# Performance work log

Hardware: AMD Instinct MI355X
Metric: run time of the kernel (lower is better)

Reference implementation:

```python
import jax, jax.numpy as jnp
import numpy as np

# dims (match init_kwargs)
T, B, N, D_OB = 256, 32, 64, 4
D_MODEL = N * D_OB            # 256
D_PE = 16
D_T = D_MODEL + D_PE          # 272 transformer width
H = 8
DH = D_T // H                 # 34
L = 2
DFF = 1024
C = 2
MAX_LEN = T
F_IN = T * D_OB               # 1024, ObservationPropagation channels


def setup_inputs() -> dict:
    key = jax.random.key(0)
    ks = jax.random.split(key, 24)
    g = lambda k, shp: 0.02 * jax.random.normal(k, shp, dtype=jnp.float32)
    return {
        "x": jax.random.normal(ks[0], (T, B, N), dtype=jnp.float32),
        "times": jnp.sort(jax.random.uniform(ks[1], (T, B), dtype=jnp.float32) * MAX_LEN, axis=0),
        "lengths": jax.random.randint(ks[2], (B,), MAX_LEN // 2, MAX_LEN + 1),
        "R_u": g(ks[3], (1, N * D_OB)),
        "Wv1": g(ks[4], (F_IN, F_IN)), "bv1": g(ks[5], (F_IN,)),
        "Wv2": g(ks[6], (F_IN, F_IN)), "bv2": g(ks[7], (F_IN,)),
        "qkv_w": g(ks[8], (L, D_T, 3 * D_T)), "qkv_b": g(ks[9], (L, 3 * D_T)),
        "out_w": g(ks[10], (L, D_T, D_T)), "out_b": g(ks[11], (L, D_T)),
        "ln1_w": jnp.ones((L, D_T), jnp.float32), "ln1_b": jnp.zeros((L, D_T), jnp.float32),
        "ln2_w": jnp.ones((L, D_T), jnp.float32), "ln2_b": jnp.zeros((L, D_T), jnp.float32),
        "ffn_w1": g(ks[12], (L, D_T, DFF)), "ffn_b1": g(ks[13], (L, DFF)),
        "ffn_w2": g(ks[14], (L, DFF, D_T)), "ffn_b2": g(ks[15], (L, D_T)),
        "mlp_w1": g(ks[16], (D_T, D_T)), "mlp_b1": g(ks[17], (D_T,)),
        "mlp_w2": g(ks[18], (D_T, C)), "mlp_b2": g(ks[19], (C,)),
    }


def _pos_encode(times):
    # PositionalEncodingTF: timescales = max_len ** linspace(0,1,d_pe//2)
    scales = MAX_LEN ** np.linspace(0.0, 1.0, D_PE // 2)
    st = times[..., None] / jnp.asarray(scales, times.dtype)  # [T,B,8]
    return jnp.concatenate([jnp.sin(st), jnp.cos(st)], axis=-1)  # [T,B,16]


def _segment_softmax(w, seg, num_segments):
    m = jax.ops.segment_max(w, seg, num_segments=num_segments)
    e = jnp.exp(w - m[seg])
    s = jax.ops.segment_sum(e, seg, num_segments=num_segments)
    return e / s[seg]


def _ob_propagate(xn, src, tgt, edge_w, Wv, bv):
    """Batched ObservationPropagation (use_beta=False, decompose=False).
    xn: [B,N,F]; messages = relu(lin_value(x_src)) * softmax(edge_w per target);
    scatter-add at targets. Returns (out, pre-softmax alpha == edge_w)."""
    gamma = _segment_softmax(edge_w, tgt, N)              # [E]
    value = jax.nn.relu(xn @ Wv + bv)                     # [B,N,F] (linear commutes with gather)
    msg = value[:, src, :] * gamma[None, :, None]         # [B,E,F] -- dominant memory traffic
    out = jnp.zeros_like(xn).at[:, tgt, :].add(msg)       # segment-sum at target nodes
    return out, edge_w


def _ln(x, w, b):
    mu = jnp.mean(x, axis=-1, keepdims=True)
    var = jnp.mean((x - mu) ** 2, axis=-1, keepdims=True)
    return (x - mu) / jnp.sqrt(var + 1e-5) * w + b


def _encoder_layer(xt, key_pad, qkv_w, qkv_b, out_w, out_b, ln1_w, ln1_b, ln2_w, ln2_b, w1, b1, w2, b2):
    # xt: [T,B,D_T]; key_pad: [B,T] True = padded. Post-norm torch TransformerEncoderLayer, relu, no dropout.
    Tt, Bb, _ = xt.shape
    q, k, v = jnp.split(xt @ qkv_w + qkv_b, 3, axis=-1)
    to_h = lambda t: t.reshape(Tt, Bb, H, DH).transpose(1, 2, 0, 3)  # [B,H,T,dh]
    scores = jnp.einsum("bhqd,bhkd->bhqk", to_h(q), to_h(k)) / jnp.sqrt(jnp.asarray(DH, xt.dtype))
    scores = jnp.where(key_pad[:, None, None, :], -jnp.inf, scores)
    attn = jax.nn.softmax(scores, axis=-1)
    o = jnp.einsum("bhqk,bhkd->bhqd", attn, to_h(v)).transpose(2, 0, 1, 3).reshape(Tt, Bb, D_T)
    xt = _ln(xt + o @ out_w + out_b, ln1_w, ln1_b)
    ff = jax.nn.relu(xt @ w1 + b1) @ w2 + b2
    return _ln(xt + ff, ln2_w, ln2_b)


def _forward(x, times, lengths, R_u, Wv1, bv1, Wv2, bv2, qkv_w, qkv_b, out_w, out_b,
             ln1_w, ln1_b, ln2_w, ln2_b, ffn_w1, ffn_b1, ffn_w2, ffn_b2,
             mlp_w1, mlp_b1, mlp_w2, mlp_b2):
    Bb = x.shape[1]
    # observation embedding: repeat each sensor d_ob times, scale by R_u, relu
    h = jax.nn.relu(jnp.repeat(x, D_OB, axis=-1) * R_u)          # [T,B,N*d_ob]
    pe = _pos_encode(times)                                      # [T,B,16]
    key_pad = jnp.arange(T)[None, :] >= lengths[:, None]         # [B,T]
    # reshape to per-sensor node features: [B, N, T*d_ob]
    xn = h.reshape(T, Bb, N, D_OB).transpose(1, 2, 0, 3).reshape(Bb, N, F_IN)
    # dense all-pairs graph (global_structure = ones); torch.nonzero order is row-major
    src = jnp.repeat(jnp.arange(N), N)   # edge_index[0]
    tgt = jnp.tile(jnp.arange(N), N)     # edge_index[1] (aggregation index)
    ew = jnp.ones((N * N,), x.dtype)
    xn, ew2 = _ob_propagate(xn, src, tgt, ew, Wv1, bv1)
    xn, _ = _ob_propagate(xn, src, tgt, ew2, Wv2, bv2)
    out = xn.reshape(Bb, N, T, D_OB).transpose(2, 0, 1, 3).reshape(T, Bb, N * D_OB)
    out = jnp.concatenate([out, pe], axis=2)                     # [T,B,272]
    for l in range(L):
        out = _encoder_layer(out, key_pad, qkv_w[l], qkv_b[l], out_w[l], out_b[l],
                             ln1_w[l], ln1_b[l], ln2_w[l], ln2_b[l],
                             ffn_w1[l], ffn_b1[l], ffn_w2[l], ffn_b2[l])
    keep = (~key_pad).T[:, :, None].astype(out.dtype)            # [T,B,1]
    agg = jnp.sum(out * keep, axis=0) / (lengths[:, None].astype(out.dtype) + 1.0)
    hid = jax.nn.relu(agg @ mlp_w1 + mlp_b1)
    logits = hid @ mlp_w2 + mlp_b2
    return jax.nn.softmax(logits, axis=1)                        # [B,C]


def reference(x, times, lengths, R_u, Wv1, bv1, Wv2, bv2, qkv_w, qkv_b, out_w, out_b,
              ln1_w, ln1_b, ln2_w, ln2_b, ffn_w1, ffn_b1, ffn_w2, ffn_b2,
              mlp_w1, mlp_b1, mlp_w2, mlp_b2):
    return _forward(x, times, lengths, R_u, Wv1, bv1, Wv2, bv2, qkv_w, qkv_b, out_w, out_b,
                    ln1_w, ln1_b, ln2_w, ln2_b, ffn_w1, ffn_b1, ffn_w2, ffn_b2,
                    mlp_w1, mlp_b1, mlp_w2, mlp_b2)
```

## Files before the change

kernel.cpp:

```cpp
#include <hip/hip_runtime.h>
#include <math.h>

#define T_DIM 256
#define B_DIM 32
#define N_DIM 64
#define F_INF 1024
#define D_T 272
#define D_TP 288
#define H_DIM 8
#define DH_DIM 34
#define DFF_DIM 1024

typedef unsigned int uint;
typedef short bf16x8 __attribute__((ext_vector_type(8)));
typedef float f32x4 __attribute__((ext_vector_type(4)));

__device__ __forceinline__ ushort f2bf(float f) {
    uint u = __float_as_uint(f);
    uint r = (u + 0x7fffu + ((u >> 16) & 1u)) >> 16;
    return (ushort)r;
}
__device__ __forceinline__ float bf2f(ushort u) {
    return __uint_as_float(((uint)u) << 16);
}

__global__ void xn_kernel(const float* __restrict__ x, const float* __restrict__ Ru,
                          ushort* __restrict__ xn) {
    int idx = blockIdx.x * blockDim.x + threadIdx.x;
    if (idx >= B_DIM * N_DIM * F_INF) return;
    int f = idx & 1023;
    int bn = idx >> 10;
    int n = bn & 63;
    int b = bn >> 6;
    int t = f >> 2;
    int d = f & 3;
    float v = x[(t * B_DIM + b) * N_DIM + n] * Ru[(n << 2) + d];
    xn[idx] = f2bf(fmaxf(v, 0.0f));
}

struct WT {
    int tstart[11];
    const float* src[10];
    ushort* dst[10];
    int K[10];
    int N[10];
    int Kp[10];
    int ntn[10];
};
__global__ __launch_bounds__(256) void wconv_tiled(WT s) {
    int tile = blockIdx.x;
    int seg = 0;
    while (seg < 9 && tile >= s.tstart[seg + 1]) ++seg;
    int ti = tile - s.tstart[seg];
    int ntn = s.ntn[seg];
    int tk = ti / ntn, tn = ti - tk * ntn;
    int N = s.N[seg], Kp = s.Kp[seg];
    __shared__ float t[16][17];
    int ty = threadIdx.x >> 4, tx = threadIdx.x & 15;
    t[ty][tx] = s.src[seg][(size_t)(tk * 16 + ty) * N + tn * 16 + tx];
    __syncthreads();
    s.dst[seg][(size_t)(tn * 16 + ty) * Kp + tk * 16 + tx] = f2bf(t[tx][ty]);
}

template <int ACT, int OUT_MODE>
__global__ __launch_bounds__(256) void gemm_mfma(const ushort* __restrict__ A,
                                                 const ushort* __restrict__ Bt,
                                                 const float* __restrict__ bias,
                                                 void* __restrict__ Cout,
                                                 int M, int N, int K, int Kstride) {
    __shared__ ushort As[4][64 * 32];
    __shared__ ushort Bs[4][128 * 32];
    const int tid = threadIdx.x;
    const int m0 = (OUT_MODE == 3) ? 0 : blockIdx.y * 64;
    const int n0 = blockIdx.x * 128;
    if (OUT_MODE == 3) {
        A += (size_t)blockIdx.y * K;
        Bt += (size_t)blockIdx.y * K;
    }
    const int w = tid >> 6, lane = tid & 63;
    const int wr = w >> 1, wc = w & 1;
    const int lr = lane & 15, lk = lane >> 4;

    const int ns = K >> 5;

    const int ra = w * 16 + (lane >> 2);
    const int ca = (((lane & 3) ^ ((ra >> 1) & 3)) << 3);
    int gma = m0 + ra; if (gma > M - 1) gma = M - 1;
    const ushort* gA = &A[(size_t)gma * Kstride + ca];
    const int rb0 = w * 32 + (lane >> 2);
    const int cb0 = (((lane & 3) ^ ((rb0 >> 1) & 3)) << 3);
    const int rb1 = rb0 + 16;
    const int cb1 = (((lane & 3) ^ ((rb1 >> 1) & 3)) << 3);
    int gnb0 = n0 + rb0; if (gnb0 > N - 1) gnb0 = N - 1;
    int gnb1 = n0 + rb1; if (gnb1 > N - 1) gnb1 = N - 1;
    const ushort* gB0 = &Bt[(size_t)gnb0 * Kstride + cb0];
    const ushort* gB1 = &Bt[(size_t)gnb1 * Kstride + cb1];

    f32x4 acc[2][4];
#pragma unroll
    for (int i = 0; i < 2; ++i)
#pragma unroll
        for (int j = 0; j < 4; ++j) acc[i][j] = (f32x4){0.f, 0.f, 0.f, 0.f};

    auto stage = [&](int buf, int s) {
        const int k0 = s << 5;
        __builtin_amdgcn_global_load_lds(
            (const __attribute__((address_space(1))) void*)(gA + k0),
            (__attribute__((address_space(3))) void*)(&As[buf][w * 512]), 16, 0, 0);
        __builtin_amdgcn_global_load_lds(
            (const __attribute__((address_space(1))) void*)(gB0 + k0),
            (__attribute__((address_space(3))) void*)(&Bs[buf][w * 1024]), 16, 0, 0);
        __builtin_amdgcn_global_load_lds(
            (const __attribute__((address_space(1))) void*)(gB1 + k0),
            (__attribute__((address_space(3))) void*)(&Bs[buf][w * 1024 + 512]), 16, 0, 0);
    };

    stage(0, 0);
    stage(1, 1);
    stage(2, 2);
    asm volatile("s_waitcnt vmcnt(6)" ::: "memory");
    __builtin_amdgcn_sched_barrier(0);
    __builtin_amdgcn_s_barrier();
    __builtin_amdgcn_sched_barrier(0);

    int cur = 0;
    for (int s = 0; s < ns; ++s) {
        int stg = (cur + 3) & 3;
        if (s + 3 < ns) stage(stg, s + 3);

        bf16x8 af[2], bf[4];
#pragma unroll
        for (int mt = 0; mt < 2; ++mt) {
            int row = wr * 32 + mt * 16 + lr;
            int ch = lk ^ ((row >> 1) & 3);
            af[mt] = *reinterpret_cast<const bf16x8*>(&As[cur][row * 32 + ch * 8]);
        }
#pragma unroll
        for (int nt = 0; nt < 4; ++nt) {
            int row = wc * 64 + nt * 16 + lr;
            int ch = lk ^ ((row >> 1) & 3);
            bf[nt] = *reinterpret_cast<const bf16x8*>(&Bs[cur][row * 32 + ch * 8]);
        }
        __builtin_amdgcn_s_setprio(1);
#pragma unroll
        for (int mt = 0; mt < 2; ++mt)
#pragma unroll
            for (int nt = 0; nt < 4; ++nt)
                acc[mt][nt] = __builtin_amdgcn_mfma_f32_16x16x32_bf16(
                    af[mt], bf[nt], acc[mt][nt], 0, 0, 0);
        __builtin_amdgcn_s_setprio(0);

        if (s + 1 < ns) {
            if (s + 3 < ns)
                asm volatile("s_waitcnt vmcnt(6)" ::: "memory");
            else if (s + 2 < ns)
                asm volatile("s_waitcnt vmcnt(3)" ::: "memory");
            else
                asm volatile("s_waitcnt vmcnt(0)" ::: "memory");
            __builtin_amdgcn_sched_barrier(0);
            __builtin_amdgcn_s_barrier();
            __builtin_amdgcn_sched_barrier(0);
        }
        cur = (cur + 1) & 3;
    }

#pragma unroll
    for (int nt = 0; nt < 4; ++nt) {
        int col = n0 + wc * 64 + nt * 16 + lr;
        if (col >= N) continue;
        float bv = (OUT_MODE == 3) ? 0.f : bias[col];
        int g = 0, dcol = 0;
        if (OUT_MODE == 2) { g = col / 34; dcol = col - g * 34; }
#pragma unroll
        for (int mt = 0; mt < 2; ++mt) {
#pragma unroll
            for (int r = 0; r < 4; ++r) {
                int row = m0 + wr * 32 + mt * 16 + lk * 4 + r;
                if (row >= M) continue;
                float v = acc[mt][nt][r] + bv;
                if (ACT == 1) v = fmaxf(v, 0.0f);
                if (OUT_MODE == 0)
                    ((float*)Cout)[(size_t)row * N + col] = v;
                else if (OUT_MODE == 1)
                    ((ushort*)Cout)[(size_t)row * N + col] = f2bf(v);
                else if (OUT_MODE == 2)
                    ((ushort*)Cout)[(size_t)row * 960 + g * 40 + dcol] = f2bf(v);
                else
                    ((float*)Cout)[(size_t)(blockIdx.y * M + row) * N + col] = v;
            }
        }
    }
}

__global__ __launch_bounds__(256) void reduce_s1_kernel(const ushort* __restrict__ val1,
                                                        ushort* __restrict__ s1) {
    int idx = blockIdx.x * 256 + threadIdx.x;
    if (idx >= B_DIM * 128) return;
    int b = idx >> 7;
    int g0 = (idx & 127) << 3;
    const ushort* base = val1 + (size_t)(b << 6) * F_INF + g0;
    float s[8] = {0.f, 0.f, 0.f, 0.f, 0.f, 0.f, 0.f, 0.f};
    for (int n = 0; n < 64; ++n) {
        bf16x8 v = *reinterpret_cast<const bf16x8*>(base + (size_t)n * F_INF);
#pragma unroll
        for (int e = 0; e < 8; ++e) s[e] += bf2f((ushort)v[e]);
    }
    ushort o[8];
#pragma unroll
    for (int e = 0; e < 8; ++e) o[e] = f2bf(s[e] * (1.0f / 64.0f));
    *reinterpret_cast<uint4*>(&s1[(size_t)idx * 8]) = *reinterpret_cast<uint4*>(o);
}

__global__ __launch_bounds__(256) void reduce_p2_kernel(const float* __restrict__ part,
                                                        const float* __restrict__ bv2,
                                                        float* __restrict__ out2) {
    int idx = blockIdx.x * 256 + threadIdx.x;
    if (idx >= B_DIM * F_INF) return;
    int g = idx & 1023;
    float s = bv2[g];
#pragma unroll
    for (int ks = 0; ks < 4; ++ks) s += part[(size_t)ks * B_DIM * F_INF + idx];
    out2[idx] = fmaxf(s, 0.f);
}

__global__ void seq_kernel(const float* __restrict__ out2, const float* __restrict__ times,
                           ushort* __restrict__ seq) {
    int idx = blockIdx.x * blockDim.x + threadIdx.x;
    if (idx >= T_DIM * B_DIM * D_TP) return;
    int c = idx % D_TP;
    int tb = idx / D_TP;
    float v;
    if (c < 256) {
        v = out2[(tb % B_DIM) * 1024 + ((tb / B_DIM) << 2) + (c & 3)];
    } else if (c < 272) {
        int s = c - 256;
        int sc = (s < 8) ? s : s - 8;
        float arg = times[tb] * exp2f(-8.0f * (float)sc * (1.0f / 7.0f));
        v = (s < 8) ? sinf(arg) : cosf(arg);
    } else {
        v = 0.f;
    }
    seq[idx] = f2bf(v);
}

struct PadPtrs {
    uint* wt[6];
    int nrows[6];
};
__global__ void init_pads_kernel(uint* __restrict__ qkvb, uint* __restrict__ x1,
                                 uint* __restrict__ attno, PadPtrs p) {
    const int TB = T_DIM * B_DIM;
    int idx = blockIdx.x * blockDim.x + threadIdx.x;
    if (idx < TB * 8) {
        int row = idx >> 3, q = idx & 7;
        x1[(size_t)row * 144 + 136 + q] = 0;
        attno[(size_t)row * 144 + 136 + q] = 0;
        return;
    }
    idx -= TB * 8;
    if (idx < TB * 72) {
        int row = idx / 72;
        int r = idx - row * 72;
        int g = r / 3, q = r - g * 3;
        qkvb[(size_t)row * 480 + g * 20 + 17 + q] = 0;
        return;
    }
    idx -= TB * 72;
#pragma unroll
    for (int sgi = 0; sgi < 6; ++sgi) {
        int cnt = p.nrows[sgi] * 8;
        if (idx < cnt) {
            int row = idx >> 3, q = idx & 7;
            p.wt[sgi][(size_t)row * 144 + 136 + q] = 0;
            return;
        }
        idx -= cnt;
    }
}

__global__ __launch_bounds__(256) void attn_mfma(const ushort* __restrict__ qkv,
                                                 const int* __restrict__ lengths,
                                                 ushort* __restrict__ attno) {
    const int b = blockIdx.x >> 3;
    const int h = blockIdx.x & 7;
    const int tid = threadIdx.x;
    const int w = tid >> 6, lane = tid & 63;
    const int lr = lane & 15, lk = lane >> 4;
    __shared__ ushort Ks[2][64 * 40];
    __shared__ ushort Vt[2][48 * 72];
    __shared__ ushort Ps[4][64 * 72];
    const int len = lengths[b];
    const float scale = 0.1714985851f;
    const bf16x8 zv = {0, 0, 0, 0, 0, 0, 0, 0};

    for (int i = tid; i < 2 * 8 * 72; i += 256) {
        int bb = i / 576;
        Vt[bb][40 * 72 + (i - bb * 576)] = 0;
    }

    const int srow0 = tid / 5, sch0 = tid - srow0 * 5;
    const int srow1 = (tid + 256) / 5, sch1 = (tid + 256) - srow1 * 5;
    const int sjp0 = (srow0 & 15) * 4 + (srow0 >> 4);
    const int sjp1 = (srow1 & 15) * 4 + (srow1 >> 4);
    const bool has1 = (tid < 64);
    bf16x8 kreg0, kreg1, vreg0, vreg1;

    auto LOADS = [&](int c) {
        const ushort* b0 = &qkv[(size_t)((c * 64 + srow0) * 32 + b) * 960 + h * 40];
        kreg0 = *reinterpret_cast<const bf16x8*>(b0 + 320 + sch0 * 8);
        vreg0 = *reinterpret_cast<const bf16x8*>(b0 + 640 + sch0 * 8);
        if (has1) {
            const ushort* b1 = &qkv[(size_t)((c * 64 + srow1) * 32 + b) * 960 + h * 40];
            kreg1 = *reinterpret_cast<const bf16x8*>(b1 + 320 + sch1 * 8);
            vreg1 = *reinterpret_cast<const bf16x8*>(b1 + 640 + sch1 * 8);
        }
    };
    auto WRITES = [&](int buf) {
        *reinterpret_cast<bf16x8*>(&Ks[buf][srow0 * 40 + sch0 * 8]) = kreg0;
#pragma unroll
        for (int e = 0; e < 8; ++e) Vt[buf][(sch0 * 8 + e) * 72 + sjp0] = (ushort)vreg0[e];
        if (has1) {
            *reinterpret_cast<bf16x8*>(&Ks[buf][srow1 * 40 + sch1 * 8]) = kreg1;
#pragma unroll
            for (int e = 0; e < 8; ++e) Vt[buf][(sch1 * 8 + e) * 72 + sjp1] = (ushort)vreg1[e];
        }
    };

    bf16x8 qf0[4], qf1[4];
#pragma unroll
    for (int it = 0; it < 4; ++it) {
        int t = w * 64 + it * 16 + lr;
        const ushort* qrow = &qkv[(size_t)(t * 32 + b) * 960 + h * 40];
        qf0[it] = *reinterpret_cast<const bf16x8*>(qrow + lk * 8);
        qf1[it] = (lk == 0) ? *reinterpret_cast<const bf16x8*>(qrow + 32) : zv;
    }

    f32x4 oacc[4][3];
#pragma unroll
    for (int it = 0; it < 4; ++it)
#pragma unroll
        for (int dt = 0; dt < 3; ++dt) oacc[it][dt] = (f32x4){0.f, 0.f, 0.f, 0.f};
    float m[4][4], l[4][4];
#pragma unroll
    for (int it = 0; it < 4; ++it)
#pragma unroll
        for (int r = 0; r < 4; ++r) { m[it][r] = -1e30f; l[it][r] = 0.f; }

    const int nchunks = (len + 63) >> 6;
    LOADS(0);
    WRITES(0);
    __syncthreads();

    int cur = 0;
    for (int c = 0; c < nchunks; ++c) {
        const bool pre = (c + 1 < nchunks);
        if (pre) LOADS(c + 1);

        bf16x8 kf0[4], kf1[4];
#pragma unroll
        for (int jt = 0; jt < 4; ++jt) {
            int j = jt * 16 + lr;
            kf0[jt] = *reinterpret_cast<const bf16x8*>(&Ks[cur][j * 40 + lk * 8]);
            kf1[jt] = (lk == 0) ? *reinterpret_cast<const bf16x8*>(&Ks[cur][j * 40 + 32]) : zv;
        }

        const bool tail = (c * 64 + 64 > len);
#pragma unroll
        for (int it = 0; it < 4; ++it) {
            f32x4 sacc[4];
#pragma unroll
            for (int jt = 0; jt < 4; ++jt) sacc[jt] = (f32x4){0.f, 0.f, 0.f, 0.f};
            __builtin_amdgcn_s_setprio(1);
#pragma unroll
            for (int jt = 0; jt < 4; ++jt) {
                sacc[jt] = __builtin_amdgcn_mfma_f32_16x16x32_bf16(qf0[it], kf0[jt],
                                                                   sacc[jt], 0, 0, 0);
                sacc[jt] = __builtin_amdgcn_mfma_f32_16x16x32_bf16(qf1[it], kf1[jt],
                                                                   sacc[jt], 0, 0, 0);
            }
            __builtin_amdgcn_s_setprio(0);
            float cm[4] = {-1e30f, -1e30f, -1e30f, -1e30f};
#pragma unroll
            for (int jt = 0; jt < 4; ++jt) {
                bool dead = tail && (c * 64 + jt * 16 + lr >= len);
#pragma unroll
                for (int r = 0; r < 4; ++r) {
                    float sv = dead ? -1e30f : sacc[jt][r];
                    sacc[jt][r] = sv;
                    cm[r] = fmaxf(cm[r], sv);
                }
            }
#pragma unroll
            for (int mask = 1; mask <= 8; mask <<= 1)
#pragma unroll
                for (int r = 0; r < 4; ++r) cm[r] = fmaxf(cm[r], __shfl_xor(cm[r], mask));
#pragma unroll
            for (int r = 0; r < 4; ++r) {
                float mn = fmaxf(m[it][r], cm[r]);
                float corr = __expf((m[it][r] - mn) * scale);
                m[it][r] = mn;
                l[it][r] *= corr;
#pragma unroll
                for (int dt = 0; dt < 3; ++dt) oacc[it][dt][r] *= corr;
            }
            float ls[4] = {0.f, 0.f, 0.f, 0.f};
#pragma unroll
            for (int jt = 0; jt < 4; ++jt)
#pragma unroll
                for (int r = 0; r < 4; ++r) {
                    float e = __expf((sacc[jt][r] - m[it][r]) * scale);
                    sacc[jt][r] = e;
                    ls[r] += e;
                }
#pragma unroll
            for (int mask = 1; mask <= 8; mask <<= 1)
#pragma unroll
                for (int r = 0; r < 4; ++r) ls[r] += __shfl_xor(ls[r], mask);
#pragma unroll
            for (int r = 0; r < 4; ++r) l[it][r] += ls[r];
#pragma unroll
            for (int r = 0; r < 4; ++r) {
                int i = it * 16 + lk * 4 + r;
                uint u0 = (uint)f2bf(sacc[0][r]) | ((uint)f2bf(sacc[1][r]) << 16);
                uint u1 = (uint)f2bf(sacc[2][r]) | ((uint)f2bf(sacc[3][r]) << 16);
                uint2 pk = make_uint2(u0, u1);
                *reinterpret_cast<uint2*>(&Ps[w][i * 72 + lr * 4]) = pk;
            }
        }

        bf16x8 vf[3][2], pf[4][2];
#pragma unroll
        for (int dt = 0; dt < 3; ++dt)
#pragma unroll
            for (int ks = 0; ks < 2; ++ks)
                vf[dt][ks] = *reinterpret_cast<const bf16x8*>(
                    &Vt[cur][(dt * 16 + lr) * 72 + ks * 32 + lk * 8]);
#pragma unroll
        for (int it = 0; it < 4; ++it)
#pragma unroll
            for (int ks = 0; ks < 2; ++ks)
                pf[it][ks] = *reinterpret_cast<const bf16x8*>(
                    &Ps[w][(it * 16 + lr) * 72 + ks * 32 + lk * 8]);
        __builtin_amdgcn_s_setprio(1);
#pragma unroll
        for (int it = 0; it < 4; ++it)
#pragma unroll
            for (int dt = 0; dt < 3; ++dt)
#pragma unroll
                for (int ks = 0; ks < 2; ++ks)
                    oacc[it][dt] = __builtin_amdgcn_mfma_f32_16x16x32_bf16(
                        pf[it][ks], vf[dt][ks], oacc[it][dt], 0, 0, 0);
        __builtin_amdgcn_s_setprio(0);

        if (pre) WRITES(cur ^ 1);
        __syncthreads();
        cur ^= 1;
    }

#pragma unroll
    for (int it = 0; it < 4; ++it)
#pragma unroll
        for (int r = 0; r < 4; ++r) {
            float inv = 1.0f / l[it][r];
            int t = w * 64 + it * 16 + lk * 4 + r;
            ushort* orow = &attno[(size_t)(t * 32 + b) * D_TP + h * 34];
#pragma unroll
            for (int dt = 0; dt < 3; ++dt) {
                int d = dt * 16 + lr;
                if (d < 34) orow[d] = f2bf(oacc[it][dt][r] * inv);
            }
        }
}

__global__ __launch_bounds__(256) void ln_kernel(const ushort* __restrict__ X,
                                                 const float* __restrict__ Y,
                                                 const float* __restrict__ w,
                                                 const float* __restrict__ bsh,
                                                 ushort* __restrict__ out) {
    int row = blockIdx.x * 4 + (threadIdx.x >> 6);
    int lane = threadIdx.x & 63;
    const ushort* xr = X + (size_t)row * D_TP;
    const float* yr = Y + (size_t)row * D_T;
    float v[5];
    float sum = 0.f, sumsq = 0.f;
#pragma unroll
    for (int k = 0; k < 5; ++k) {
        int c = lane + k * 64;
        float t = 0.f;
        if (c < D_T) t = bf2f(xr[c]) + yr[c];
        v[k] = t;
        sum += t;
        sumsq += t * t;
    }
#pragma unroll
    for (int off = 32; off; off >>= 1) {
        sum += __shfl_down(sum, off);
        sumsq += __shfl_down(sumsq, off);
    }
    sum = __shfl(sum, 0);
    sumsq = __shfl(sumsq, 0);
    float mu = sum * (1.0f / D_T);
    float var = sumsq * (1.0f / D_T) - mu * mu;
    float inv = 1.0f / sqrtf(var + 1e-5f);
    ushort* orow = out + (size_t)row * D_TP;
#pragma unroll
    for (int k = 0; k < 5; ++k) {
        int c = lane + k * 64;
        if (c < D_T) orow[c] = f2bf((v[k] - mu) * inv * w[c] + bsh[c]);
    }
}

__global__ __launch_bounds__(256) void pool_partial(const ushort* __restrict__ seq,
                                                    const int* __restrict__ lengths,
                                                    float* __restrict__ partial) {
    const int chunk = blockIdx.x;
    const int b = blockIdx.y;
    const int tid = threadIdx.x;
    if (tid >= 136) return;
    const int len = lengths[b];
    float s0 = 0.f, s1 = 0.f;
    int t0 = chunk * 32;
    int tmax = len - t0;
    if (tmax > 32) tmax = 32;
#pragma unroll 4
    for (int r = 0; r < tmax; ++r) {
        uint u = *reinterpret_cast<const uint*>(
            &seq[(size_t)((t0 + r) * B_DIM + b) * D_TP + tid * 2]);
        s0 += __uint_as_float(u << 16);
        s1 += __uint_as_float(u & 0xffff0000u);
    }
    float* p = &partial[(size_t)(chunk * B_DIM + b) * D_T + tid * 2];
    p[0] = s0;
    p[1] = s1;
}

__global__ __launch_bounds__(256) void head_kernel(const float* __restrict__ partial,
                                                   const int* __restrict__ lengths,
                                                   const float* __restrict__ w1,
                                                   const float* __restrict__ b1,
                                                   const float* __restrict__ w2,
                                                   const float* __restrict__ b2,
                                                   float* __restrict__ out) {
    const int b = blockIdx.x;
    const int tid = threadIdx.x;
    const int len = lengths[b];
    __shared__ float agg_s[D_T];
    __shared__ float hid[D_T];
    float inv = 1.0f / (float)(len + 1);
    for (int c = tid; c < D_T; c += 256) {
        float s = 0.f;
#pragma unroll
        for (int ch = 0; ch < 8; ++ch)
            s += partial[(size_t)(ch * B_DIM + b) * D_T + c];
        agg_s[c] = s * inv;
    }
    __syncthreads();
    for (int j = tid; j < D_T; j += 256) {
        float acc = b1[j];
        for (int k = 0; k < D_T; ++k) acc += agg_s[k] * w1[k * D_T + j];
        hid[j] = fmaxf(acc, 0.f);
    }
    __syncthreads();
    if (tid < 64) {
        float l0 = 0.f, l1 = 0.f;
        for (int k = tid; k < D_T; k += 64) {
            float hv = hid[k];
            l0 += hv * w2[k * 2 + 0];
            l1 += hv * w2[k * 2 + 1];
        }
#pragma unroll
        for (int off = 32; off; off >>= 1) {
            l0 += __shfl_down(l0, off);
            l1 += __shfl_down(l1, off);
        }
        if (tid == 0) {
            l0 += b2[0];
            l1 += b2[1];
            float mx = fmaxf(l0, l1);
            float e0 = expf(l0 - mx), e1 = expf(l1 - mx);
            float nrm = 1.0f / (e0 + e1);
            out[b * 2 + 0] = e0 * nrm;
            out[b * 2 + 1] = e1 * nrm;
        }
    }
}

extern "C" void kernel_launch(void* const* d_in, const int* in_sizes, int n_in,
                              void* d_out, int out_size, void* d_ws, size_t ws_size,
                              hipStream_t stream) {
    const float* x      = (const float*)d_in[0];
    const float* times  = (const float*)d_in[1];
    const int*   lens   = (const int*)d_in[2];
    const float* R_u    = (const float*)d_in[3];
    const float* Wv1    = (const float*)d_in[4];
    const float* bv1    = (const float*)d_in[5];
    const float* Wv2    = (const float*)d_in[6];
    const float* bv2    = (const float*)d_in[7];
    const float* qkv_w  = (const float*)d_in[8];
    const float* qkv_b  = (const float*)d_in[9];
    const float* out_w  = (const float*)d_in[10];
    const float* out_b  = (const float*)d_in[11];
    const float* ln1_w  = (const float*)d_in[12];
    const float* ln1_b  = (const float*)d_in[13];
    const float* ln2_w  = (const float*)d_in[14];
    const float* ln2_b  = (const float*)d_in[15];
    const float* ffn_w1 = (const float*)d_in[16];
    const float* ffn_b1 = (const float*)d_in[17];
    const float* ffn_w2 = (const float*)d_in[18];
    const float* ffn_b2 = (const float*)d_in[19];
    const float* mlp_w1 = (const float*)d_in[20];
    const float* mlp_b1 = (const float*)d_in[21];
    const float* mlp_w2 = (const float*)d_in[22];
    const float* mlp_b2 = (const float*)d_in[23];
    float* outp = (float*)d_out;

    char* base = (char*)d_ws;
    size_t used = 0;
    auto alloc = [&](size_t bytes) -> char* {
        char* p = base + used;
        used += (bytes + 255) & ~(size_t)255;
        return p;
    };
    const int TB = T_DIM * B_DIM;

    ushort* xn    = (ushort*)alloc((size_t)2048 * 1024 * 2);
    ushort* val1  = (ushort*)alloc((size_t)2048 * 1024 * 2);
    ushort* s1    = (ushort*)alloc((size_t)32 * 1024 * 2);
    float*  p2p   = (float*) alloc((size_t)4 * 32 * 1024 * 4);
    float*  out2  = (float*) alloc((size_t)32 * 1024 * 4);
    ushort* seq   = (ushort*)alloc((size_t)TB * D_TP * 2);
    ushort* qkvb  = (ushort*)alloc((size_t)TB * 960 * 2);
    ushort* attno = (ushort*)alloc((size_t)TB * D_TP * 2);
    float*  tmp   = (float*) alloc((size_t)TB * D_T * 4);
    ushort* x1    = (ushort*)alloc((size_t)TB * D_TP * 2);
    ushort* h1    = (ushort*)alloc((size_t)TB * DFF_DIM * 2);
    float*  ppart = (float*) alloc((size_t)8 * B_DIM * D_T * 4);
    ushort* wv1t  = (ushort*)alloc((size_t)1024 * 1024 * 2);
    ushort* wv2t  = (ushort*)alloc((size_t)1024 * 1024 * 2);
    ushort* qkvwt[2]; ushort* outwt[2]; ushort* f1wt[2]; ushort* f2wt[2];
    for (int l = 0; l < 2; ++l) {
        qkvwt[l] = (ushort*)alloc((size_t)816 * D_TP * 2);
        outwt[l] = (ushort*)alloc((size_t)272 * D_TP * 2);
        f1wt[l]  = (ushort*)alloc((size_t)1024 * D_TP * 2);
        f2wt[l]  = (ushort*)alloc((size_t)272 * 1024 * 2);
    }
    if (used > ws_size) return;

    {
        WT segs;
        const float* srcs[10] = {Wv1, Wv2,
                                 qkv_w, out_w, ffn_w1, ffn_w2,
                                 qkv_w + (size_t)272 * 816, out_w + (size_t)272 * 272,
                                 ffn_w1 + (size_t)272 * 1024, ffn_w2 + (size_t)1024 * 272};
        ushort* dsts[10] = {wv1t, wv2t, qkvwt[0], outwt[0], f1wt[0], f2wt[0],
                            qkvwt[1], outwt[1], f1wt[1], f2wt[1]};
        int Ksz[10] = {1024, 1024, 272, 272, 272, 1024, 272, 272, 272, 1024};
        int Nsz[10] = {1024, 1024, 816, 272, 1024, 272, 816, 272, 1024, 272};
        int Kpd[10] = {1024, 1024, D_TP, D_TP, D_TP, 1024, D_TP, D_TP, D_TP, 1024};
        int acc = 0;
        for (int i = 0; i < 10; ++i) {
            segs.tstart[i] = acc;
            segs.src[i] = srcs[i];
            segs.dst[i] = dsts[i];
            segs.K[i] = Ksz[i];
            segs.N[i] = Nsz[i];
            segs.Kp[i] = Kpd[i];
            segs.ntn[i] = Nsz[i] / 16;
            acc += (Ksz[i] / 16) * (Nsz[i] / 16);
        }
        segs.tstart[10] = acc;
        wconv_tiled<<<acc, 256, 0, stream>>>(segs);
    }

    {
        PadPtrs pp;
        pp.wt[0] = (uint*)qkvwt[0]; pp.nrows[0] = 816;
        pp.wt[1] = (uint*)qkvwt[1]; pp.nrows[1] = 816;
        pp.wt[2] = (uint*)outwt[0]; pp.nrows[2] = 272;
        pp.wt[3] = (uint*)outwt[1]; pp.nrows[3] = 272;
        pp.wt[4] = (uint*)f1wt[0];  pp.nrows[4] = 1024;
        pp.wt[5] = (uint*)f1wt[1];  pp.nrows[5] = 1024;
        int n = TB * 8 + TB * 72 + (816 + 816 + 272 + 272 + 1024 + 1024) * 8;
        init_pads_kernel<<<(n + 255) / 256, 256, 0, stream>>>((uint*)qkvb, (uint*)x1,
                                                              (uint*)attno, pp);
    }

    {
        int n = B_DIM * N_DIM * F_INF;
        xn_kernel<<<(n + 255) / 256, 256, 0, stream>>>(x, R_u, xn);
    }

    gemm_mfma<1, 1><<<dim3(8, 32), 256, 0, stream>>>(xn, wv1t, bv1, val1,
                                                     2048, 1024, 1024, 1024);
    reduce_s1_kernel<<<16, 256, 0, stream>>>(val1, s1);
    gemm_mfma<0, 3><<<dim3(8, 4), 256, 0, stream>>>(s1, wv2t, nullptr, p2p,
                                                    32, 1024, 256, 1024);
    reduce_p2_kernel<<<128, 256, 0, stream>>>(p2p, bv2, out2);

    {
        int n = TB * D_TP;
        seq_kernel<<<(n + 255) / 256, 256, 0, stream>>>(out2, times, seq);
    }

    for (int l = 0; l < 2; ++l) {
        const float* qb  = qkv_b + (size_t)l * 816;
        const float* ob  = out_b + (size_t)l * D_T;
        const float* l1w = ln1_w + (size_t)l * D_T;
        const float* l1b = ln1_b + (size_t)l * D_T;
        const float* l2w = ln2_w + (size_t)l * D_T;
        const float* l2b = ln2_b + (size_t)l * D_T;
        const float* f1b = ffn_b1 + (size_t)l * DFF_DIM;
        const float* f2b = ffn_b2 + (size_t)l * D_T;

        gemm_mfma<0, 2><<<dim3(7, 128), 256, 0, stream>>>(seq, qkvwt[l], qb, qkvb,
                                                          TB, 816, D_TP, D_TP);
        attn_mfma<<<B_DIM * H_DIM, 256, 0, stream>>>(qkvb, lens, attno);
        gemm_mfma<0, 0><<<dim3(3, 128), 256, 0, stream>>>(attno, outwt[l], ob, tmp,
                                                          TB, D_T, D_TP, D_TP);
        ln_kernel<<<TB / 4, 256, 0, stream>>>(seq, tmp, l1w, l1b, x1);
        gemm_mfma<1, 1><<<dim3(8, 128), 256, 0, stream>>>(x1, f1wt[l], f1b, h1,
                                                          TB, DFF_DIM, D_TP, D_TP);
        gemm_mfma<0, 0><<<dim3(3, 128), 256, 0, stream>>>(h1, f2wt[l], f2b, tmp,
                                                          TB, D_T, 1024, 1024);
        ln_kernel<<<TB / 4, 256, 0, stream>>>(x1, tmp, l2w, l2b, seq);
    }

    pool_partial<<<dim3(8, B_DIM), 256, 0, stream>>>(seq, lens, ppart);
    head_kernel<<<B_DIM, 256, 0, stream>>>(ppart, lens, mlp_w1, mlp_b1,
                                           mlp_w2, mlp_b2, outp);
}
```

Before: 323.4 us.

## Fuse residual+LayerNorm into output GEMMs and fold node-mean into first GEMM

Adds a gemm_ln kernel that computes a full 64x272 row tile per block and applies bias, residual add and LayerNorm in the epilogue. This replaces the separate fp32 tmp write and the ln_kernel pass for both the attention-out and FFN2 projections. The ObservationPropagation first GEMM gains an OUT_MODE 4 epilogue that applies ReLU and reduces over the 64 nodes into s1 directly, removing the val1 buffer and reduce_s1_kernel. The generic GEMM pipeline also drops from 4 to 3 LDS stages. In exchange, the LN-fused GEMM launches only 128 blocks with 17 accumulators each and double buffering, which may reduce occupancy and latency hiding.

```diff
diff --git a/kernel.cpp b/kernel.cpp
--- a/kernel.cpp
+++ b/kernel.cpp
@@ -68,8 +68,8 @@
                                                  const float* __restrict__ bias,
                                                  void* __restrict__ Cout,
                                                  int M, int N, int K, int Kstride) {
-    __shared__ ushort As[4][64 * 32];
-    __shared__ ushort Bs[4][128 * 32];
+    __shared__ ushort As[3][64 * 32];
+    __shared__ ushort Bs[3][128 * 32];
     const int tid = threadIdx.x;
     const int m0 = (OUT_MODE == 3) ? 0 : blockIdx.y * 64;
     const int n0 = blockIdx.x * 128;
@@ -117,16 +117,15 @@
 
     stage(0, 0);
     stage(1, 1);
-    stage(2, 2);
-    asm volatile("s_waitcnt vmcnt(6)" ::: "memory");
+    asm volatile("s_waitcnt vmcnt(3)" ::: "memory");
     __builtin_amdgcn_sched_barrier(0);
     __builtin_amdgcn_s_barrier();
     __builtin_amdgcn_sched_barrier(0);
 
     int cur = 0;
     for (int s = 0; s < ns; ++s) {
-        int stg = (cur + 3) & 3;
-        if (s + 3 < ns) stage(stg, s + 3);
+        int stg = cur + 2; if (stg >= 3) stg -= 3;
+        if (s + 2 < ns) stage(stg, s + 2);
 
         bf16x8 af[2], bf[4];
 #pragma unroll
@@ -151,9 +150,7 @@
         __builtin_amdgcn_s_setprio(0);
 
         if (s + 1 < ns) {
-            if (s + 3 < ns)
-                asm volatile("s_waitcnt vmcnt(6)" ::: "memory");
-            else if (s + 2 < ns)
+            if (s + 2 < ns)
                 asm volatile("s_waitcnt vmcnt(3)" ::: "memory");
             else
                 asm volatile("s_waitcnt vmcnt(0)" ::: "memory");
@@ -161,7 +158,36 @@
             __builtin_amdgcn_s_barrier();
             __builtin_amdgcn_sched_barrier(0);
         }
-        cur = (cur + 1) & 3;
+        cur = (cur == 2) ? 0 : cur + 1;
+    }
+
+    if (OUT_MODE == 4) {
+        __shared__ float red[2][128];
+        float part[4];
+#pragma unroll
+        for (int nt = 0; nt < 4; ++nt) {
+            int col = n0 + wc * 64 + nt * 16 + lr;
+            float bv = bias[col];
+            float s = 0.f;
+#pragma unroll
+            for (int mt = 0; mt < 2; ++mt)
+#pragma unroll
+                for (int r = 0; r < 4; ++r) s += fmaxf(acc[mt][nt][r] + bv, 0.f);
+            s += __shfl_xor(s, 16);
+            s += __shfl_xor(s, 32);
+            part[nt] = s;
+        }
+        if (lk == 0) {
+#pragma unroll
+            for (int nt = 0; nt < 4; ++nt) red[wr][wc * 64 + nt * 16 + lr] = part[nt];
+        }
+        __syncthreads();
+        if (tid < 128) {
+            float tot = red[0][tid] + red[1][tid];
+            ((ushort*)Cout)[(size_t)blockIdx.y * 1024 + n0 + tid] =
+                f2bf(tot * (1.0f / 64.0f));
+        }
+        return;
     }
 
 #pragma unroll
@@ -192,23 +218,128 @@
     }
 }
 
-__global__ __launch_bounds__(256) void reduce_s1_kernel(const ushort* __restrict__ val1,
-                                                        ushort* __restrict__ s1) {
-    int idx = blockIdx.x * 256 + threadIdx.x;
-    if (idx >= B_DIM * 128) return;
-    int b = idx >> 7;
-    int g0 = (idx & 127) << 3;
-    const ushort* base = val1 + (size_t)(b << 6) * F_INF + g0;
-    float s[8] = {0.f, 0.f, 0.f, 0.f, 0.f, 0.f, 0.f, 0.f};
-    for (int n = 0; n < 64; ++n) {
-        bf16x8 v = *reinterpret_cast<const bf16x8*>(base + (size_t)n * F_INF);
-#pragma unroll
-        for (int e = 0; e < 8; ++e) s[e] += bf2f((ushort)v[e]);
-    }
-    ushort o[8];
-#pragma unroll
-    for (int e = 0; e < 8; ++e) o[e] = f2bf(s[e] * (1.0f / 64.0f));
-    *reinterpret_cast<uint4*>(&s1[(size_t)idx * 8]) = *reinterpret_cast<uint4*>(o);
+__global__ __launch_bounds__(256) void gemm_ln(const ushort* __restrict__ A,
+                                               const ushort* __restrict__ Bt,
+                                               const float* __restrict__ bias,
+                                               const ushort* __restrict__ resid,
+                                               const float* __restrict__ lnw,
+                                               const float* __restrict__ lnb,
+                                               ushort* __restrict__ Out,
+                                               int K, int Kstride) {
+    __shared__ ushort lds[21504];
+    const int tid = threadIdx.x;
+    const int m0 = blockIdx.x * 64;
+    const int w = tid >> 6, lane = tid & 63;
+    const int lr = lane & 15, lk = lane >> 4;
+    const int ns = K >> 5;
+
+    const int ra = w * 16 + (lane >> 2);
+    const int ca = (((lane & 3) ^ ((ra >> 1) & 3)) << 3);
+    const ushort* gA = &A[(size_t)(m0 + ra) * Kstride + ca];
+
+    f32x4 acc[17];
+#pragma unroll
+    for (int t = 0; t < 17; ++t) acc[t] = (f32x4){0.f, 0.f, 0.f, 0.f};
+
+    auto stage = [&](int buf, int s) {
+        const int k0 = s << 5;
+        __builtin_amdgcn_global_load_lds(
+            (const __attribute__((address_space(1))) void*)(gA + k0),
+            (__attribute__((address_space(3))) void*)(&lds[buf * 2048 + w * 512]),
+            16, 0, 0);
+        for (int c = w; c < 17; c += 4) {
+            int row16 = c * 16 + (lane >> 2);
+            int p8 = (((lane & 3) ^ ((row16 >> 1) & 3)) << 3);
+            const ushort* src = &Bt[(size_t)row16 * Kstride + k0 + p8];
+            __builtin_amdgcn_global_load_lds(
+                (const __attribute__((address_space(1))) void*)src,
+                (__attribute__((address_space(3))) void*)(&lds[4096 + buf * 8704 + c * 512]),
+                16, 0, 0);
+        }
+    };
+
+    stage(0, 0);
+    asm volatile("s_waitcnt vmcnt(0)" ::: "memory");
+    __builtin_amdgcn_sched_barrier(0);
+    __builtin_amdgcn_s_barrier();
+    __builtin_amdgcn_sched_barrier(0);
+
+    int cur = 0;
+    for (int s = 0; s < ns; ++s) {
+        if (s + 1 < ns) stage(cur ^ 1, s + 1);
+
+        bf16x8 af;
+        {
+            int row = w * 16 + lr;
+            int ch = lk ^ ((row >> 1) & 3);
+            af = *reinterpret_cast<const bf16x8*>(&lds[cur * 2048 + row * 32 + ch * 8]);
+        }
+        __builtin_amdgcn_s_setprio(1);
+#pragma unroll
+        for (int t = 0; t < 17; ++t) {
+            int row = t * 16 + lr;
+            int ch = lk ^ ((row >> 1) & 3);
+            bf16x8 bf = *reinterpret_cast<const bf16x8*>(
+                &lds[4096 + cur * 8704 + row * 32 + ch * 8]);
+            acc[t] = __builtin_amdgcn_mfma_f32_16x16x32_bf16(af, bf, acc[t], 0, 0, 0);
+        }
+        __builtin_amdgcn_s_setprio(0);
+
+        if (s + 1 < ns) {
+            asm volatile("s_waitcnt vmcnt(0)" ::: "memory");
+            __builtin_amdgcn_sched_barrier(0);
+            __builtin_amdgcn_s_barrier();
+            __builtin_amdgcn_sched_barrier(0);
+        }
+        cur ^= 1;
+    }
+
+    __syncthreads();
+    for (int i = tid; i < 64 * 34; i += 256) {
+        int row = i / 34, c8 = i - row * 34;
+        *reinterpret_cast<uint4*>(&lds[row * 272 + c8 * 8]) =
+            *reinterpret_cast<const uint4*>(&resid[(size_t)(m0 + row) * D_TP + c8 * 8]);
+    }
+    __syncthreads();
+
+    float sum[4] = {0.f, 0.f, 0.f, 0.f}, sq[4] = {0.f, 0.f, 0.f, 0.f};
+#pragma unroll
+    for (int t = 0; t < 17; ++t) {
+        int col = t * 16 + lr;
+        float bv = bias[col];
+#pragma unroll
+        for (int r = 0; r < 4; ++r) {
+            int row = w * 16 + lk * 4 + r;
+            float v = acc[t][r] + bv + bf2f(lds[row * 272 + col]);
+            acc[t][r] = v;
+            sum[r] += v;
+            sq[r] += v * v;
+        }
+    }
+#pragma unroll
+    for (int mask = 1; mask <= 8; mask <<= 1)
+#pragma unroll
+        for (int r = 0; r < 4; ++r) {
+            sum[r] += __shfl_xor(sum[r], mask);
+            sq[r] += __shfl_xor(sq[r], mask);
+        }
+    float mu[4], inv[4];
+#pragma unroll
+    for (int r = 0; r < 4; ++r) {
+        mu[r] = sum[r] * (1.0f / D_T);
+        float var = sq[r] * (1.0f / D_T) - mu[r] * mu[r];
+        inv[r] = 1.0f / sqrtf(var + 1e-5f);
+    }
+#pragma unroll
+    for (int t = 0; t < 17; ++t) {
+        int col = t * 16 + lr;
+        float wv = lnw[col], bb = lnb[col];
+#pragma unroll
+        for (int r = 0; r < 4; ++r) {
+            int row = m0 + w * 16 + lk * 4 + r;
+            Out[(size_t)row * D_TP + col] = f2bf((acc[t][r] - mu[r]) * inv[r] * wv + bb);
+        }
+    }
 }
 
 __global__ __launch_bounds__(256) void reduce_p2_kernel(const float* __restrict__ part,
@@ -470,44 +601,6 @@
                 if (d < 34) orow[d] = f2bf(oacc[it][dt][r] * inv);
             }
         }
-}
-
-__global__ __launch_bounds__(256) void ln_kernel(const ushort* __restrict__ X,
-                                                 const float* __restrict__ Y,
-                                                 const float* __restrict__ w,
-                                                 const float* __restrict__ bsh,
-                                                 ushort* __restrict__ out) {
-    int row = blockIdx.x * 4 + (threadIdx.x >> 6);
-    int lane = threadIdx.x & 63;
-    const ushort* xr = X + (size_t)row * D_TP;
-    const float* yr = Y + (size_t)row * D_T;
-    float v[5];
-    float sum = 0.f, sumsq = 0.f;
-#pragma unroll
-    for (int k = 0; k < 5; ++k) {
-        int c = lane + k * 64;
-        float t = 0.f;
-        if (c < D_T) t = bf2f(xr[c]) + yr[c];
-        v[k] = t;
-        sum += t;
-        sumsq += t * t;
-    }
-#pragma unroll
-    for (int off = 32; off; off >>= 1) {
-        sum += __shfl_down(sum, off);
-        sumsq += __shfl_down(sumsq, off);
-    }
-    sum = __shfl(sum, 0);
-    sumsq = __shfl(sumsq, 0);
-    float mu = sum * (1.0f / D_T);
-    float var = sumsq * (1.0f / D_T) - mu * mu;
-    float inv = 1.0f / sqrtf(var + 1e-5f);
-    ushort* orow = out + (size_t)row * D_TP;
-#pragma unroll
-    for (int k = 0; k < 5; ++k) {
-        int c = lane + k * 64;
-        if (c < D_T) orow[c] = f2bf((v[k] - mu) * inv * w[c] + bsh[c]);
-    }
 }
 
 __global__ __launch_bounds__(256) void pool_partial(const ushort* __restrict__ seq,
@@ -624,14 +717,12 @@
     const int TB = T_DIM * B_DIM;
 
     ushort* xn    = (ushort*)alloc((size_t)2048 * 1024 * 2);
-    ushort* val1  = (ushort*)alloc((size_t)2048 * 1024 * 2);
     ushort* s1    = (ushort*)alloc((size_t)32 * 1024 * 2);
     float*  p2p   = (float*) alloc((size_t)4 * 32 * 1024 * 4);
     float*  out2  = (float*) alloc((size_t)32 * 1024 * 4);
     ushort* seq   = (ushort*)alloc((size_t)TB * D_TP * 2);
     ushort* qkvb  = (ushort*)alloc((size_t)TB * 960 * 2);
     ushort* attno = (ushort*)alloc((size_t)TB * D_TP * 2);
-    float*  tmp   = (float*) alloc((size_t)TB * D_T * 4);
     ushort* x1    = (ushort*)alloc((size_t)TB * D_TP * 2);
     ushort* h1    = (ushort*)alloc((size_t)TB * DFF_DIM * 2);
     float*  ppart = (float*) alloc((size_t)8 * B_DIM * D_T * 4);
@@ -690,9 +781,8 @@
         xn_kernel<<<(n + 255) / 256, 256, 0, stream>>>(x, R_u, xn);
     }
 
-    gemm_mfma<1, 1><<<dim3(8, 32), 256, 0, stream>>>(xn, wv1t, bv1, val1,
+    gemm_mfma<1, 4><<<dim3(8, 32), 256, 0, stream>>>(xn, wv1t, bv1, s1,
                                                      2048, 1024, 1024, 1024);
-    reduce_s1_kernel<<<16, 256, 0, stream>>>(val1, s1);
     gemm_mfma<0, 3><<<dim3(8, 4), 256, 0, stream>>>(s1, wv2t, nullptr, p2p,
                                                     32, 1024, 256, 1024);
     reduce_p2_kernel<<<128, 256, 0, stream>>>(p2p, bv2, out2);
@@ -715,14 +805,12 @@
         gemm_mfma<0, 2><<<dim3(7, 128), 256, 0, stream>>>(seq, qkvwt[l], qb, qkvb,
                                                           TB, 816, D_TP, D_TP);
         attn_mfma<<<B_DIM * H_DIM, 256, 0, stream>>>(qkvb, lens, attno);
-        gemm_mfma<0, 0><<<dim3(3, 128), 256, 0, stream>>>(attno, outwt[l], ob, tmp,
-                                                          TB, D_T, D_TP, D_TP);
-        ln_kernel<<<TB / 4, 256, 0, stream>>>(seq, tmp, l1w, l1b, x1);
+        gemm_ln<<<128, 256, 0, stream>>>(attno, outwt[l], ob, seq, l1w, l1b, x1,
+                                         D_TP, D_TP);
         gemm_mfma<1, 1><<<dim3(8, 128), 256, 0, stream>>>(x1, f1wt[l], f1b, h1,
                                                           TB, DFF_DIM, D_TP, D_TP);
-        gemm_mfma<0, 0><<<dim3(3, 128), 256, 0, stream>>>(h1, f2wt[l], f2b, tmp,
-                                                          TB, D_T, 1024, 1024);
-        ln_kernel<<<TB / 4, 256, 0, stream>>>(x1, tmp, l2w, l2b, seq);
+        gemm_ln<<<128, 256, 0, stream>>>(h1, f2wt[l], f2b, x1, l2w, l2b, seq,
+                                         1024, 1024);
     }
 
     pool_partial<<<dim3(8, B_DIM), 256, 0, stream>>>(seq, lens, ppart);
```

Result: faster. 287.7 us (-11.1%).
